# Optimization experiments

Measured on AMD Instinct MI355X. Metric: run time of the kernel, lower is better.

The kernel has to match this reference:

```python
import jax, jax.numpy as jnp
import numpy as np

B, T, H, E, D, K = 4, 4096, 2048, 8, 1024, 2

def setup_inputs() -> dict:
    key = jax.random.key(0)
    ks = jax.random.split(key, 7)
    x  = jax.random.normal(ks[0], (B, T, H), dtype=jnp.float32)
    Wr = jax.random.normal(ks[1], (H, E), dtype=jnp.float32) * (1.0 / np.sqrt(H))
    br = jnp.zeros((E,), dtype=jnp.float32)
    We = jax.random.normal(ks[2], (E, H, D), dtype=jnp.float32) * (1.0 / np.sqrt(H))
    be = jnp.zeros((E, D), dtype=jnp.float32)
    Wc = jax.random.normal(ks[3], (D, H), dtype=jnp.float32) * (1.0 / np.sqrt(D))
    bc = jnp.zeros((H,), dtype=jnp.float32)
    return {"x": x, "Wr": Wr, "br": br, "We": We, "be": be, "Wc": Wc, "bc": bc}

def reference(x, Wr, br, We, be, Wc, bc):
    # Router: [B,T,H] @ [H,E] -> [B,T,E]
    router_logits = jnp.einsum('bth,he->bte', x, Wr) + br
    scores = jax.nn.softmax(router_logits, axis=-1)
    # top-k over experts (sorted descending, like torch.topk)
    topk_scores, topk_idx = jax.lax.top_k(scores, K)  # [B,T,K]
    # Dense all-expert linear: [B,T,E,D]
    expert_outs = jnp.einsum('bth,ehd->bted', x, We) + be
    # Gather the chosen experts per token: [B,T,K,D]
    gather_idx = jnp.broadcast_to(topk_idx[..., None], (B, T, K, D))
    chosen = jnp.take_along_axis(expert_outs, gather_idx, axis=2)
    # Weighted sum over top-k: [B,T,D]
    weighted = jnp.sum(chosen * topk_scores[..., None], axis=2)
    # Combine: [B,T,D] @ [D,H] -> [B,T,H]
    return jnp.einsum('btd,dh->bth', weighted, Wc) + bc
```

## Files before the change

### kernel.cpp

```cpp
#include <hip/hip_runtime.h>
#include <hip/hip_bf16.h>

typedef float f32x4 __attribute__((ext_vector_type(4)));
typedef short bf16x8 __attribute__((ext_vector_type(8)));

#define M_NT 16
#define M_OFF 17
#define M_TBL 32
#define MAX_TILES 264
#define NCHUNK 1024

__device__ __forceinline__ void gload16(const void* g, void* l) {
  __builtin_amdgcn_global_load_lds(
      (const __attribute__((address_space(1))) void*)g,
      (__attribute__((address_space(3))) void*)l, 16, 0, 0);
}

__device__ __forceinline__ float bf2f(unsigned short u) {
  union { unsigned int i; float f; } v; v.i = ((unsigned int)u) << 16; return v.f;
}
__device__ __forceinline__ unsigned short f2bf(float f) {
  __hip_bfloat16 h = __float2bfloat16(f);
  return __builtin_bit_cast(unsigned short, h);
}

#define CBAR() do { asm volatile("" ::: "memory"); __builtin_amdgcn_s_barrier(); asm volatile("" ::: "memory"); } while (0)
#define VMC4() asm volatile("s_waitcnt vmcnt(4)" ::: "memory")
#define VMC0() asm volatile("s_waitcnt vmcnt(0)" ::: "memory")

__global__ __launch_bounds__(256) void prep_kernel(
    const float* __restrict__ x, const float* __restrict__ Wr,
    const float* __restrict__ br, unsigned short* __restrict__ xbf,
    float* __restrict__ scores, int* __restrict__ idx,
    int* __restrict__ blk_hist,
    const float* __restrict__ We, unsigned short* __restrict__ WeT,
    const float* __restrict__ Wc, unsigned short* __restrict__ WcT) {
  __shared__ float tile[32][33];
  __shared__ int cnt[8];
  int blk = blockIdx.x;
  int tid = threadIdx.x;
  if (blk < NCHUNK) {
    int lane = tid & 63, w = tid >> 6;
    if (tid < 8) cnt[tid] = 0;
    __syncthreads();
    int t0 = blk * 16 + w * 4;
    const float* xr = x + (size_t)t0 * 2048;
    unsigned short* xo = xbf + (size_t)t0 * 2048;
    float acc[4][8] = {};
#pragma unroll
    for (int j = 0; j < 8; ++j) {
      int h0 = j * 256 + lane * 4;
      float4 xv[4];
#pragma unroll
      for (int t = 0; t < 4; ++t) xv[t] = *(const float4*)(xr + (size_t)t * 2048 + h0);
#pragma unroll
      for (int t = 0; t < 4; ++t) {
        ushort4 p;
        p.x = f2bf(xv[t].x); p.y = f2bf(xv[t].y);
        p.z = f2bf(xv[t].z); p.w = f2bf(xv[t].w);
        *(ushort4*)(xo + (size_t)t * 2048 + h0) = p;
      }
      const float4* wp = (const float4*)(Wr + (size_t)h0 * 8);
#pragma unroll
      for (int c = 0; c < 4; ++c) {
        float4 w0 = wp[2 * c], w1 = wp[2 * c + 1];
        float xc0 = (c == 0) ? xv[0].x : (c == 1) ? xv[0].y : (c == 2) ? xv[0].z : xv[0].w;
        float xc1 = (c == 0) ? xv[1].x : (c == 1) ? xv[1].y : (c == 2) ? xv[1].z : xv[1].w;
        float xc2 = (c == 0) ? xv[2].x : (c == 1) ? xv[2].y : (c == 2) ? xv[2].z : xv[2].w;
        float xc3 = (c == 0) ? xv[3].x : (c == 1) ? xv[3].y : (c == 2) ? xv[3].z : xv[3].w;
        acc[0][0] += xc0 * w0.x; acc[0][1] += xc0 * w0.y; acc[0][2] += xc0 * w0.z; acc[0][3] += xc0 * w0.w;
        acc[0][4] += xc0 * w1.x; acc[0][5] += xc0 * w1.y; acc[0][6] += xc0 * w1.z; acc[0][7] += xc0 * w1.w;
        acc[1][0] += xc1 * w0.x; acc[1][1] += xc1 * w0.y; acc[1][2] += xc1 * w0.z; acc[1][3] += xc1 * w0.w;
        acc[1][4] += xc1 * w1.x; acc[1][5] += xc1 * w1.y; acc[1][6] += xc1 * w1.z; acc[1][7] += xc1 * w1.w;
        acc[2][0] += xc2 * w0.x; acc[2][1] += xc2 * w0.y; acc[2][2] += xc2 * w0.z; acc[2][3] += xc2 * w0.w;
        acc[2][4] += xc2 * w1.x; acc[2][5] += xc2 * w1.y; acc[2][6] += xc2 * w1.z; acc[2][7] += xc2 * w1.w;
        acc[3][0] += xc3 * w0.x; acc[3][1] += xc3 * w0.y; acc[3][2] += xc3 * w0.z; acc[3][3] += xc3 * w0.w;
        acc[3][4] += xc3 * w1.x; acc[3][5] += xc3 * w1.y; acc[3][6] += xc3 * w1.z; acc[3][7] += xc3 * w1.w;
      }
    }
#pragma unroll
    for (int t = 0; t < 4; ++t)
#pragma unroll
      for (int e = 0; e < 8; ++e)
#pragma unroll
        for (int off = 32; off > 0; off >>= 1)
          acc[t][e] += __shfl_xor(acc[t][e], off);
    if (lane < 4) {
      int t = t0 + lane;
      float l[8];
#pragma unroll
      for (int e = 0; e < 8; ++e) {
        float v = (lane == 0) ? acc[0][e] : (lane == 1) ? acc[1][e]
                : (lane == 2) ? acc[2][e] : acc[3][e];
        l[e] = v + br[e];
      }
      float mx = l[0];
#pragma unroll
      for (int e = 1; e < 8; ++e) mx = fmaxf(mx, l[e]);
      float se = 0.f;
#pragma unroll
      for (int e = 0; e < 8; ++e) se += __expf(l[e] - mx);
      float inv = 1.f / se;
      int e1 = 0; float b1 = l[0];
#pragma unroll
      for (int e = 1; e < 8; ++e) if (l[e] > b1) { b1 = l[e]; e1 = e; }
      int e2 = -1; float b2 = -1e30f;
#pragma unroll
      for (int e = 0; e < 8; ++e) if (e != e1 && l[e] > b2) { b2 = l[e]; e2 = e; }
      idx[2 * t] = e1; idx[2 * t + 1] = e2;
      scores[2 * t] = __expf(b1 - mx) * inv;
      scores[2 * t + 1] = __expf(b2 - mx) * inv;
      atomicAdd(&cnt[e1], 1);
      atomicAdd(&cnt[e2], 1);
    }
    __syncthreads();
    if (tid < 8) blk_hist[blk * 8 + tid] = cnt[tid];
  } else if (blk < NCHUNK + 16384) {
    int i2 = blk - NCHUNK;
    int b = i2 >> 11, rem = i2 & 2047;
    int r0 = (rem >> 5) * 32, c0 = (rem & 31) * 32;
    const float* src = We + (size_t)b * 2048 * 1024;
    unsigned short* dst = WeT + (size_t)b * 2048 * 1024;
    int tx = tid & 31, ty = tid >> 5;
#pragma unroll
    for (int i = 0; i < 32; i += 8)
      tile[ty + i][tx] = src[(size_t)(r0 + ty + i) * 1024 + c0 + tx];
    __syncthreads();
#pragma unroll
    for (int i = 0; i < 32; i += 8)
      dst[(size_t)(c0 + ty + i) * 2048 + r0 + tx] = f2bf(tile[tx][ty + i]);
  } else {
    int i2 = blk - NCHUNK - 16384;
    int r0 = (i2 >> 6) * 32, c0 = (i2 & 63) * 32;
    int tx = tid & 31, ty = tid >> 5;
#pragma unroll
    for (int i = 0; i < 32; i += 8)
      tile[ty + i][tx] = Wc[(size_t)(r0 + ty + i) * 2048 + c0 + tx];
    __syncthreads();
#pragma unroll
    for (int i = 0; i < 32; i += 8)
      WcT[(size_t)(c0 + ty + i) * 1024 + r0 + tx] = f2bf(tile[tx][ty + i]);
  }
}

__global__ __launch_bounds__(512) void scan_kernel(
    const int* __restrict__ blk_hist, int* __restrict__ chunk_base,
    int* __restrict__ meta, int* __restrict__ rowlist) {
  __shared__ int stot[8], soff[8], stbase[8];
  int tid = threadIdx.x, lane = tid & 63, e = tid >> 6;
  int running = 0;
  for (int g = 0; g < NCHUNK / 64; ++g) {
    int c = g * 64 + lane;
    int v = blk_hist[c * 8 + e];
    int orig = v;
#pragma unroll
    for (int off = 1; off < 64; off <<= 1) {
      int n = __shfl_up(v, off);
      if (lane >= off) v += n;
    }
    chunk_base[c * 8 + e] = running + v - orig;
    running += __shfl(v, 63);
  }
  if (lane == 0) stot[e] = running;
  __syncthreads();
  if (tid == 0) {
    int off = 0, nt = 0;
    for (int ee = 0; ee < 8; ++ee) {
      meta[M_OFF + ee] = off; soff[ee] = off;
      int tiles = (stot[ee] + 127) >> 7;
      stbase[ee] = nt;
      nt += tiles;
      off += tiles << 7;
    }
    meta[M_NT] = nt;
  }
  __syncthreads();
  int4* tbl = (int4*)(meta + M_TBL);
  for (int ee = 0; ee < 8; ++ee) {
    int c = stot[ee], tiles = (c + 127) >> 7;
    for (int t = tid; t < tiles; t += 512)
      tbl[stbase[ee] + t] = make_int4(ee, soff[ee] + t * 128, min(128, c - t * 128), 0);
    int end = tiles << 7;
    for (int i = c + tid; i < end; i += 512) rowlist[soff[ee] + i] = 0;
  }
}

__global__ void scatter_kernel(const int* __restrict__ idx,
                               const int* __restrict__ chunk_base,
                               const int* __restrict__ meta,
                               int* __restrict__ rowlist) {
  int c = blockIdx.x, lane = threadIdx.x;
  int entry = c * 32 + lane;
  int e = (lane < 32) ? idx[entry] : -1;
#pragma unroll
  for (int ee = 0; ee < 8; ++ee) {
    unsigned long long m = __ballot(e == ee);
    if (e == ee) {
      int rank = __popcll(m & ((1ull << lane) - 1));
      rowlist[meta[M_OFF + ee] + chunk_base[c * 8 + ee] + rank] = entry;
    }
  }
}


#define RD_FRAGS(BUFB) do { \
  _Pragma("unroll") for (int m_ = 0; m_ < 4; ++m_) \
    av[m_] = *(const bf16x8*)(aP + (BUFB) + m_ * 1024); \
  _Pragma("unroll") for (int n_ = 0; n_ < 4; ++n_) \
    bv[n_] = *(const bf16x8*)(bP + (BUFB) + n_ * 1024); \
} while (0)

#define MFMA16() do { \
  _Pragma("unroll") for (int m_ = 0; m_ < 4; ++m_) \
  _Pragma("unroll") for (int n_ = 0; n_ < 4; ++n_) \
    acc[m_][n_] = __builtin_amdgcn_mfma_f32_16x16x32_bf16(av[m_], bv[n_], acc[m_][n_], 0, 0, 0); \
} while (0)

#define STAGE(BUFB, KOFF) do { \
  gload16(pA0 + (KOFF), dA + (BUFB)); \
  gload16(pA1 + (KOFF), dA + (BUFB) + 4096); \
  gload16(pB0 + (KOFF), dB + (BUFB)); \
  gload16(pB1 + (KOFF), dB + (BUFB) + 4096); \
} while (0)

__global__ __launch_bounds__(256, 4) void expert_gemm(
    const unsigned short* __restrict__ xbf,
    const unsigned short* __restrict__ WeT,
    const float* __restrict__ be,
    const float* __restrict__ scores,
    const int* __restrict__ rowlist,
    const int* __restrict__ meta,
    unsigned short* __restrict__ z) {
  __shared__ char smem[32768];
  __shared__ int lrows[128];
  int nt = meta[M_NT];
  int flat = blockIdx.y * 8 + blockIdx.x;
  int work = (flat & 7) * MAX_TILES + (flat >> 3);
  int tileid = work >> 3, nb = work & 7;
  if (tileid >= nt) return;
  int4 tt = ((const int4*)(meta + M_TBL))[tileid];
  int e = tt.x, base = tt.y, valid = tt.z;
  int n0 = nb * 128;
  int tid = threadIdx.x, lane = tid & 63, w = tid >> 6;
  if (tid < 128) lrows[tid] = rowlist[base + tid];
  __syncthreads();
  int wm = w >> 1, wn = w & 1;
  int fl = lane & 15, q = lane >> 4;
  int rA = tid >> 2;
  int sl = ((tid & 3) ^ ((rA >> 1) & 3)) * 16;
  const char* pA0 = (const char*)xbf + (size_t)(lrows[rA] >> 1) * 4096 + sl;
  const char* pA1 = (const char*)xbf + (size_t)(lrows[rA + 64] >> 1) * 4096 + sl;
  const char* pB0 = (const char*)WeT + ((size_t)e * 1024 + n0 + rA) * 4096 + sl;
  const char* pB1 = (const char*)WeT + ((size_t)e * 1024 + n0 + rA + 64) * 4096 + sl;
  char* dA = smem + tid * 16;
  char* dB = smem + 8192 + tid * 16;
  int swz = ((fl >> 1) & 3) << 4;
  const char* aP = smem + (wm * 64 + fl) * 64 + ((q * 16) ^ swz);
  const char* bP = smem + 8192 + (wn * 64 + fl) * 64 + ((q * 16) ^ swz);
  STAGE(0, 0); STAGE(16384, 64);
  VMC4(); CBAR();
  f32x4 acc[4][4] = {};
  bf16x8 av[4], bv[4];
  const int NT = 64;
  for (int t2 = 0; t2 < NT; t2 += 2) {
    int koff = t2 * 64;
    RD_FRAGS(0);
    MFMA16();
    CBAR();
    if (t2 + 2 < NT) { STAGE(0, koff + 128); VMC4(); } else { VMC0(); }
    CBAR();
    RD_FRAGS(16384);
    MFMA16();
    CBAR();
    if (t2 + 3 < NT) { STAGE(16384, koff + 192); VMC4(); } else { VMC0(); }
    CBAR();
  }
  float bev[4];
#pragma unroll
  for (int nc = 0; nc < 4; ++nc)
    bev[nc] = be[e * 1024 + n0 + wn * 64 + nc * 16 + fl];
#pragma unroll
  for (int mi = 0; mi < 4; ++mi) {
    int rowbase = wm * 64 + mi * 16 + q * 4;
#pragma unroll
    for (int r = 0; r < 4; ++r) {
      int row = rowbase + r;
      if (row < valid) {
        int entry = lrows[row];
        float s = scores[entry];
        unsigned short* zr = z + (size_t)entry * 1024 + n0 + wn * 64 + fl;
#pragma unroll
        for (int nc = 0; nc < 4; ++nc)
          zr[nc * 16] = f2bf((acc[mi][nc][r] + bev[nc]) * s);
      }
    }
  }
}

__global__ __launch_bounds__(256, 4) void combine_gemm(
    const unsigned short* __restrict__ y,
    const unsigned short* __restrict__ WcT,
    const float* __restrict__ bc,
    float* __restrict__ out) {
  __shared__ char smem[32768];
  int flat = blockIdx.y * 8 + blockIdx.x;
  int work = (flat & 7) * 256 + (flat >> 3);
  int mt = work >> 4, nb = work & 15;
  int m0 = mt * 128, n0 = nb * 128;
  int tid = threadIdx.x, lane = tid & 63, w = tid >> 6;
  int wm = w >> 1, wn = w & 1;
  int fl = lane & 15, q = lane >> 4;
  int rA = tid >> 2;
  int sl = ((tid & 3) ^ ((rA >> 1) & 3)) * 16;
  const char* pA0 = (const char*)y + (size_t)(m0 + rA) * 2048 + sl;
  const char* pA1 = (const char*)y + (size_t)(m0 + rA + 64) * 2048 + sl;
  const char* pB0 = (const char*)WcT + (size_t)(n0 + rA) * 2048 + sl;
  const char* pB1 = (const char*)WcT + (size_t)(n0 + rA + 64) * 2048 + sl;
  char* dA = smem + tid * 16;
  char* dB = smem + 8192 + tid * 16;
  int swz = ((fl >> 1) & 3) << 4;
  const char* aP = smem + (wm * 64 + fl) * 64 + ((q * 16) ^ swz);
  const char* bP = smem + 8192 + (wn * 64 + fl) * 64 + ((q * 16) ^ swz);
  STAGE(0, 0); STAGE(16384, 64);
  VMC4(); CBAR();
  f32x4 acc[4][4] = {};
  bf16x8 av[4], bv[4];
  const int NT = 32;
  for (int t2 = 0; t2 < NT; t2 += 2) {
    int koff = t2 * 64;
    RD_FRAGS(0);
    MFMA16();
    CBAR();
    if (t2 + 2 < NT) { STAGE(0, koff + 128); VMC4(); } else { VMC0(); }
    CBAR();
    RD_FRAGS(16384);
    MFMA16();
    CBAR();
    if (t2 + 3 < NT) { STAGE(16384, koff + 192); VMC4(); } else { VMC0(); }
    CBAR();
  }
  float bcv[4];
#pragma unroll
  for (int nc = 0; nc < 4; ++nc)
    bcv[nc] = bc[n0 + wn * 64 + nc * 16 + fl];
#pragma unroll
  for (int mi = 0; mi < 4; ++mi) {
    int rowbase = m0 + wm * 64 + mi * 16 + q * 4;
#pragma unroll
    for (int r = 0; r < 4; ++r) {
      float* orow = out + (size_t)(rowbase + r) * 2048 + n0 + wn * 64 + fl;
#pragma unroll
      for (int nc = 0; nc < 4; ++nc)
        orow[nc * 16] = acc[mi][nc][r] + bcv[nc];
    }
  }
}

__global__ void wsum_kernel(const unsigned short* __restrict__ z,
                            unsigned short* __restrict__ y) {
  size_t i = ((size_t)blockIdx.x * 256 + threadIdx.x) * 8;
  size_t t = i >> 10, d = i & 1023;
  int4 za = *(const int4*)(z + (t * 2) * 1024 + d);
  int4 zb = *(const int4*)(z + (t * 2 + 1) * 1024 + d);
  int4 r;
  const unsigned short* pa = (const unsigned short*)&za;
  const unsigned short* pb = (const unsigned short*)&zb;
  unsigned short* pr = (unsigned short*)&r;
#pragma unroll
  for (int j = 0; j < 8; ++j) pr[j] = f2bf(bf2f(pa[j]) + bf2f(pb[j]));
  *(int4*)(y + i) = r;
}

extern "C" void kernel_launch(void* const* d_in, const int* in_sizes, int n_in,
                              void* d_out, int out_size, void* d_ws, size_t ws_size,
                              hipStream_t stream) {
  const float* x  = (const float*)d_in[0];
  const float* Wr = (const float*)d_in[1];
  const float* br = (const float*)d_in[2];
  const float* We = (const float*)d_in[3];
  const float* be = (const float*)d_in[4];
  const float* Wc = (const float*)d_in[5];
  const float* bc = (const float*)d_in[6];
  float* out = (float*)d_out;

  char* ws = (char*)d_ws;
  size_t o = 0;
  auto alloc = [&](size_t b) {
    char* p = ws + o;
    o = (o + b + 255) & ~(size_t)255;
    return p;
  };
  unsigned short* xbf = (unsigned short*)alloc(16384UL * 2048 * 2);
  unsigned short* WeT = (unsigned short*)alloc(8UL * 1024 * 2048 * 2);
  unsigned short* WcT = (unsigned short*)alloc(2048UL * 1024 * 2);
  unsigned short* z   = (unsigned short*)alloc(32768UL * 1024 * 2);
  unsigned short* yw  = (unsigned short*)alloc(16384UL * 1024 * 2);
  float* scores = (float*)alloc(32768UL * 4);
  int* idx      = (int*)alloc(32768UL * 4);
  int* rowlist  = (int*)alloc(36864UL * 4);
  int* meta     = (int*)alloc(8192);
  int* blk_hist = (int*)alloc(NCHUNK * 8 * 4);
  int* chunk_base = (int*)alloc(NCHUNK * 8 * 4);
  (void)ws_size; (void)in_sizes; (void)n_in; (void)out_size;

  hipLaunchKernelGGL(prep_kernel, dim3(NCHUNK + 16384 + 2048), dim3(256), 0, stream,
                     x, Wr, br, xbf, scores, idx, blk_hist, We, WeT, Wc, WcT);
  hipLaunchKernelGGL(scan_kernel, dim3(1), dim3(512), 0, stream, blk_hist, chunk_base, meta, rowlist);
  hipLaunchKernelGGL(scatter_kernel, dim3(NCHUNK), dim3(64), 0, stream, idx, chunk_base, meta, rowlist);
  hipLaunchKernelGGL(expert_gemm, dim3(8, MAX_TILES), dim3(256), 0, stream,
                     xbf, WeT, be, scores, rowlist, meta, z);
  hipLaunchKernelGGL(wsum_kernel, dim3(8192), dim3(256), 0, stream, z, yw);
  hipLaunchKernelGGL(combine_gemm, dim3(8, 256), dim3(256), 0, stream, yw, WcT, bc, out);
}
```

Baseline: 375.5 us.

## Replace double-buffered LDS pipeline with single-buffer load-sync-compute loop

Both the expert and combine GEMMs drop the two-stage LDS ping-pong with manual vmcnt waits. Each k-step now loads its tile into a single 16KB buffer, synchronizes, and then computes. This halves the shared memory per block and simplifies synchronization, which could raise occupancy. The cost is that global-load latency is no longer overlapped with MFMA work.

```diff
diff --git a/kernel.cpp b/kernel.cpp
--- a/kernel.cpp
+++ b/kernel.cpp
@@ -23,10 +23,6 @@
   __hip_bfloat16 h = __float2bfloat16(f);
   return __builtin_bit_cast(unsigned short, h);
 }
-
-#define CBAR() do { asm volatile("" ::: "memory"); __builtin_amdgcn_s_barrier(); asm volatile("" ::: "memory"); } while (0)
-#define VMC4() asm volatile("s_waitcnt vmcnt(4)" ::: "memory")
-#define VMC0() asm volatile("s_waitcnt vmcnt(0)" ::: "memory")
 
 __global__ __launch_bounds__(256) void prep_kernel(
     const float* __restrict__ x, const float* __restrict__ Wr,
@@ -203,11 +199,11 @@
 }
 
 
-#define RD_FRAGS(BUFB) do { \
+#define RD_FRAGS() do { \
   _Pragma("unroll") for (int m_ = 0; m_ < 4; ++m_) \
-    av[m_] = *(const bf16x8*)(aP + (BUFB) + m_ * 1024); \
+    av[m_] = *(const bf16x8*)(aP + m_ * 1024); \
   _Pragma("unroll") for (int n_ = 0; n_ < 4; ++n_) \
-    bv[n_] = *(const bf16x8*)(bP + (BUFB) + n_ * 1024); \
+    bv[n_] = *(const bf16x8*)(bP + n_ * 1024); \
 } while (0)
 
 #define MFMA16() do { \
@@ -216,11 +212,11 @@
     acc[m_][n_] = __builtin_amdgcn_mfma_f32_16x16x32_bf16(av[m_], bv[n_], acc[m_][n_], 0, 0, 0); \
 } while (0)
 
-#define STAGE(BUFB, KOFF) do { \
-  gload16(pA0 + (KOFF), dA + (BUFB)); \
-  gload16(pA1 + (KOFF), dA + (BUFB) + 4096); \
-  gload16(pB0 + (KOFF), dB + (BUFB)); \
-  gload16(pB1 + (KOFF), dB + (BUFB) + 4096); \
+#define STAGE(KOFF) do { \
+  gload16(pA0 + (KOFF), dA); \
+  gload16(pA1 + (KOFF), dA + 4096); \
+  gload16(pB0 + (KOFF), dB); \
+  gload16(pB1 + (KOFF), dB + 4096); \
 } while (0)
 
 __global__ __launch_bounds__(256, 4) void expert_gemm(
@@ -231,7 +227,7 @@
     const int* __restrict__ rowlist,
     const int* __restrict__ meta,
     unsigned short* __restrict__ z) {
-  __shared__ char smem[32768];
+  __shared__ char smem[16384];
   __shared__ int lrows[128];
   int nt = meta[M_NT];
   int flat = blockIdx.y * 8 + blockIdx.x;
@@ -257,23 +253,15 @@
   int swz = ((fl >> 1) & 3) << 4;
   const char* aP = smem + (wm * 64 + fl) * 64 + ((q * 16) ^ swz);
   const char* bP = smem + 8192 + (wn * 64 + fl) * 64 + ((q * 16) ^ swz);
-  STAGE(0, 0); STAGE(16384, 64);
-  VMC4(); CBAR();
   f32x4 acc[4][4] = {};
   bf16x8 av[4], bv[4];
   const int NT = 64;
-  for (int t2 = 0; t2 < NT; t2 += 2) {
-    int koff = t2 * 64;
-    RD_FRAGS(0);
+  for (int t = 0; t < NT; ++t) {
+    STAGE(t * 64);
+    __syncthreads();
+    RD_FRAGS();
     MFMA16();
-    CBAR();
-    if (t2 + 2 < NT) { STAGE(0, koff + 128); VMC4(); } else { VMC0(); }
-    CBAR();
-    RD_FRAGS(16384);
-    MFMA16();
-    CBAR();
-    if (t2 + 3 < NT) { STAGE(16384, koff + 192); VMC4(); } else { VMC0(); }
-    CBAR();
+    __syncthreads();
   }
   float bev[4];
 #pragma unroll
@@ -302,7 +290,7 @@
     const unsigned short* __restrict__ WcT,
     const float* __restrict__ bc,
     float* __restrict__ out) {
-  __shared__ char smem[32768];
+  __shared__ char smem[16384];
   int flat = blockIdx.y * 8 + blockIdx.x;
   int work = (flat & 7) * 256 + (flat >> 3);
   int mt = work >> 4, nb = work & 15;
@@ -321,23 +309,15 @@
   int swz = ((fl >> 1) & 3) << 4;
   const char* aP = smem + (wm * 64 + fl) * 64 + ((q * 16) ^ swz);
   const char* bP = smem + 8192 + (wn * 64 + fl) * 64 + ((q * 16) ^ swz);
-  STAGE(0, 0); STAGE(16384, 64);
-  VMC4(); CBAR();
   f32x4 acc[4][4] = {};
   bf16x8 av[4], bv[4];
   const int NT = 32;
-  for (int t2 = 0; t2 < NT; t2 += 2) {
-    int koff = t2 * 64;
-    RD_FRAGS(0);
+  for (int t = 0; t < NT; ++t) {
+    STAGE(t * 64);
+    __syncthreads();
+    RD_FRAGS();
     MFMA16();
-    CBAR();
-    if (t2 + 2 < NT) { STAGE(0, koff + 128); VMC4(); } else { VMC0(); }
-    CBAR();
-    RD_FRAGS(16384);
-    MFMA16();
-    CBAR();
-    if (t2 + 3 < NT) { STAGE(16384, koff + 192); VMC4(); } else { VMC0(); }
-    CBAR();
+    __syncthreads();
   }
   float bcv[4];
 #pragma unroll
```

Result: slower. 391.3 us (+4.2%).
